# Performance work log

Hardware: AMD Instinct MI355X
Metric: run time of the kernel (lower is better)

## Reference

```python
import jax, jax.numpy as jnp
import numpy as np

B, T, H = 16, 2048, 1024
L_ORDER, R_ORDER = 1, 1
K = L_ORDER + R_ORDER + 1
THRESH = 1.0


def _alphas(hidden, conv_w, conv_b, lin_w, lin_b):
    # hidden: [B, T, H]
    context = jnp.swapaxes(hidden, 1, 2)  # [B, H, T]
    q = jnp.pad(context, ((0, 0), (0, 0), (L_ORDER, R_ORDER)))  # ConstantPad1d
    mem = jax.lax.conv_general_dilated(
        q, conv_w, (1,), 'VALID',
        dimension_numbers=('NCH', 'OIH', 'NCH'),
        feature_group_count=conv_w.shape[0])  # depthwise conv, groups=idim
    mem = mem + conv_b[None, :, None]
    out = jnp.swapaxes(mem + context, 1, 2)  # [B, T, H] (dropout = identity, eval)
    out = jax.nn.relu(out)
    out = out @ lin_w.T + lin_b  # [B, T, 1]
    return jax.nn.sigmoid(out)[..., 0]  # [B, T]


def _cif_scan(hidden, alphas, threshold):
    # sequential integrate-and-fire over time, vectorized over batch via lax.scan
    b, t, h = hidden.shape

    def step(carry, xs):
        integrate, frame = carry          # [B], [B, H]
        alpha, h_t = xs                   # [B], [B, H]
        dist = 1.0 - integrate            # distribution_completion
        integrate = integrate + alpha
        fires_t = integrate
        fire = integrate >= threshold
        integrate = jnp.where(fire, integrate - 1.0, integrate)
        cur = jnp.where(fire, dist, alpha)
        rem = alpha - cur
        frame = frame + cur[:, None] * h_t
        frames_t = frame
        frame = jnp.where(fire[:, None], rem[:, None] * h_t, frame)
        return (integrate, frame), (fires_t, frames_t)

    init = (jnp.zeros((b,), hidden.dtype), jnp.zeros((b, h), hidden.dtype))
    xs = (jnp.swapaxes(alphas, 0, 1), jnp.swapaxes(hidden, 0, 1))
    _, (fires, frames) = jax.lax.scan(step, init, xs)
    return jnp.swapaxes(frames, 0, 1), jnp.swapaxes(fires, 0, 1)  # [B,T,H], [B,T]


def _gather_fired(frames, fires, threshold, max_label_len):
    # per-batch select frames where fires>=threshold, pad to max_label_len
    b, t, h = frames.shape
    mask = fires >= threshold                         # [B, T]
    rank = jnp.cumsum(mask.astype(jnp.int32), axis=1) - 1
    idx = jnp.where(mask, rank, max_label_len)        # invalid -> dummy row
    out = jnp.zeros((b, max_label_len + 1, h), frames.dtype)
    out = out.at[jnp.arange(b)[:, None], idx].add(
        jnp.where(mask[..., None], frames, 0.0))
    return out[:, :max_label_len]


def setup_inputs() -> dict:
    key = jax.random.key(0)
    k1, k2, k3, k4 = jax.random.split(key, 4)
    hidden = jax.random.normal(k1, (B, T, H), jnp.float32)
    conv_w = jax.random.normal(k2, (H, 1, K), jnp.float32) / np.sqrt(K)
    conv_b = jax.random.normal(k3, (H,), jnp.float32) * 0.01
    lin_w = jax.random.normal(k4, (1, H), jnp.float32) / np.sqrt(H)
    lin_b = jnp.zeros((1,), jnp.float32)
    return {"hidden": hidden, "conv_w": conv_w, "conv_b": conv_b,
            "lin_w": lin_w, "lin_b": lin_b}


def reference(hidden, conv_w, conv_b, lin_w, lin_b):
    alphas = _alphas(hidden, conv_w, conv_b, lin_w, lin_b)  # [B, T]
    cif_length = alphas.sum(-1)                             # [B]
    frames, fires = _cif_scan(hidden, alphas, THRESH)
    # data-dependent output length (matches torch: round(alphas.sum(-1)).max())
    max_label_len = int(jnp.round(cif_length).astype(jnp.int32).max())
    cif_output = _gather_fired(frames, fires, THRESH, max_label_len)
    return cif_output, cif_length, fires
```

## Files before the change

### kernel.cpp

```cpp
#include <hip/hip_runtime.h>
#include <math.h>

#define B_ 16
#define T_ 2048
#define H_ 1024
#define TPB 32
#define KPB 8

typedef float f32x4_t __attribute__((ext_vector_type(4)));

__device__ __forceinline__ void ntstore4(float* p, float4 v) {
    f32x4_t w = { v.x, v.y, v.z, v.w };
    __builtin_nontemporal_store(w, (f32x4_t*)p);
}

__global__ __launch_bounds__(256) void k1_alphas(
    const float* __restrict__ hidden, const float* __restrict__ conv_w,
    const float* __restrict__ conv_b, const float* __restrict__ lin_w,
    const float* __restrict__ lin_b, float* __restrict__ alphas)
{
    const int tile = blockIdx.x & (T_ / TPB - 1);
    const int b    = blockIdx.x / (T_ / TPB);
    const int tid  = threadIdx.x;
    const int h0   = tid * 4;

    float w0[4], w1[4], w2[4];
    {
        const float4* cw = (const float4*)(conv_w + (size_t)h0 * 3);
        float4 c0 = cw[0], c1 = cw[1], c2 = cw[2];
        w0[0] = c0.x; w1[0] = c0.y; w2[0] = c0.z;
        w0[1] = c0.w; w1[1] = c1.x; w2[1] = c1.y;
        w0[2] = c1.z; w1[2] = c1.w; w2[2] = c2.x;
        w0[3] = c2.y; w1[3] = c2.z; w2[3] = c2.w;
    }
    const float4 cb = *(const float4*)(conv_b + h0);
    const float4 lw = *(const float4*)(lin_w + h0);
    const float  lb = lin_b[0];

    const size_t base = ((size_t)b * T_) * H_ + h0;
    const int t0 = tile * TPB;
    const float4 zero4 = make_float4(0.f, 0.f, 0.f, 0.f);

    float4 prev = (t0 > 0) ? *(const float4*)(hidden + base + (size_t)(t0 - 1) * H_)
                           : zero4;
    float4 curr = *(const float4*)(hidden + base + (size_t)t0 * H_);
    float4 buf0 = *(const float4*)(hidden + base + (size_t)(t0 + 1) * H_);
    float4 buf1 = *(const float4*)(hidden + base + (size_t)(t0 + 2) * H_);
    float4 buf2 = *(const float4*)(hidden + base + (size_t)(t0 + 3) * H_);
    float4 buf3 = *(const float4*)(hidden + base + (size_t)(t0 + 4) * H_);

    __shared__ float lds[4][TPB];
    const int wave = tid >> 6;
    const int lane = tid & 63;

    #pragma unroll
    for (int tt = 0; tt < TPB; ++tt) {
        float4 next;
        const int tp = t0 + tt + 5;
        switch (tt & 3) {
        case 0: next = buf0;
                buf0 = (tp < T_) ? *(const float4*)(hidden + base + (size_t)tp * H_) : zero4;
                break;
        case 1: next = buf1;
                buf1 = (tp < T_) ? *(const float4*)(hidden + base + (size_t)tp * H_) : zero4;
                break;
        case 2: next = buf2;
                buf2 = (tp < T_) ? *(const float4*)(hidden + base + (size_t)tp * H_) : zero4;
                break;
        default: next = buf3;
                buf3 = (tp < T_) ? *(const float4*)(hidden + base + (size_t)tp * H_) : zero4;
                break;
        }

        float p = 0.f, v;
        v = fmaf(w0[0], prev.x, fmaf(w1[0], curr.x, fmaf(w2[0], next.x, cb.x + curr.x)));
        p = fmaf(fmaxf(v, 0.f), lw.x, p);
        v = fmaf(w0[1], prev.y, fmaf(w1[1], curr.y, fmaf(w2[1], next.y, cb.y + curr.y)));
        p = fmaf(fmaxf(v, 0.f), lw.y, p);
        v = fmaf(w0[2], prev.z, fmaf(w1[2], curr.z, fmaf(w2[2], next.z, cb.z + curr.z)));
        p = fmaf(fmaxf(v, 0.f), lw.z, p);
        v = fmaf(w0[3], prev.w, fmaf(w1[3], curr.w, fmaf(w2[3], next.w, cb.w + curr.w)));
        p = fmaf(fmaxf(v, 0.f), lw.w, p);
        #pragma unroll
        for (int m = 32; m; m >>= 1) p += __shfl_xor(p, m);
        if (lane == 0) lds[wave][tt] = p;
        prev = curr; curr = next;
    }
    __syncthreads();
    if (tid < TPB) {
        float s = lds[0][tid] + lds[1][tid] + lds[2][tid] + lds[3][tid] + lb;
        alphas[(size_t)b * T_ + t0 + tid] = 1.f / (1.f + expf(-s));
    }
}

__global__ __launch_bounds__(256) void k2_scan_coef(
    const float* __restrict__ alphas, float* __restrict__ fires,
    float* __restrict__ wgt,
    int* __restrict__ fire_pos, int* __restrict__ n_fires,
    float* __restrict__ cif_length, int Lpad)
{
    const int b = blockIdx.x;
    const int tid = threadIdx.x;
    const size_t base = (size_t)b * T_;

    __shared__ float sA[T_];
    __shared__ float sF[T_];

    {
        const int i = tid * 8;
        *(float4*)(sA + i)     = *(const float4*)(alphas + base + i);
        *(float4*)(sA + i + 4) = *(const float4*)(alphas + base + i + 4);
    }
    __syncthreads();

    if (tid == 0) {
        float4 a0 = *(const float4*)(sA + 0);
        float4 a1 = *(const float4*)(sA + 4);
        float4 a2 = *(const float4*)(sA + 8);
        float4 a3 = *(const float4*)(sA + 12);
        float I = 0.f;
        for (int t = 0; t < T_; t += 16) {
            const int tn = (t + 16 < T_) ? t + 16 : 0;
            float4 b0 = *(const float4*)(sA + tn);
            float4 b1 = *(const float4*)(sA + tn + 4);
            float4 b2 = *(const float4*)(sA + tn + 8);
            float4 b3 = *(const float4*)(sA + tn + 12);

            float4 f0, f1, f2, f3;
            I += a0.x; f0.x = I; I = __builtin_amdgcn_fractf(I);
            I += a0.y; f0.y = I; I = __builtin_amdgcn_fractf(I);
            I += a0.z; f0.z = I; I = __builtin_amdgcn_fractf(I);
            I += a0.w; f0.w = I; I = __builtin_amdgcn_fractf(I);
            I += a1.x; f1.x = I; I = __builtin_amdgcn_fractf(I);
            I += a1.y; f1.y = I; I = __builtin_amdgcn_fractf(I);
            I += a1.z; f1.z = I; I = __builtin_amdgcn_fractf(I);
            I += a1.w; f1.w = I; I = __builtin_amdgcn_fractf(I);
            I += a2.x; f2.x = I; I = __builtin_amdgcn_fractf(I);
            I += a2.y; f2.y = I; I = __builtin_amdgcn_fractf(I);
            I += a2.z; f2.z = I; I = __builtin_amdgcn_fractf(I);
            I += a2.w; f2.w = I; I = __builtin_amdgcn_fractf(I);
            I += a3.x; f3.x = I; I = __builtin_amdgcn_fractf(I);
            I += a3.y; f3.y = I; I = __builtin_amdgcn_fractf(I);
            I += a3.z; f3.z = I; I = __builtin_amdgcn_fractf(I);
            I += a3.w; f3.w = I; I = __builtin_amdgcn_fractf(I);

            *(float4*)(sF + t)      = f0;
            *(float4*)(sF + t + 4)  = f1;
            *(float4*)(sF + t + 8)  = f2;
            *(float4*)(sF + t + 12) = f3;
            a0 = b0; a1 = b1; a2 = b2; a3 = b3;
        }
    }
    __syncthreads();

    const int t0 = tid * 8;
    float a[8], f[8];
    #pragma unroll
    for (int j = 0; j < 8; ++j) { a[j] = sA[t0 + j]; f[j] = sF[t0 + j]; }
    const float fprev = (t0 == 0) ? 0.f : sF[t0 - 1];

    ntstore4(fires + base + t0,     make_float4(f[0], f[1], f[2], f[3]));
    ntstore4(fires + base + t0 + 4, make_float4(f[4], f[5], f[6], f[7]));

    float w[16];
    bool fr[8];
    float asum = 0.f;
    int cnt = 0;
    #pragma unroll
    for (int j = 0; j < 8; ++j) {
        float fp = (j == 0) ? fprev : f[j - 1];
        float Iprev = __builtin_amdgcn_fractf(fp);
        fr[j] = (f[j] >= 1.f);
        const float dist = 1.f - Iprev;
        const float cu = fr[j] ? dist : a[j];
        const float re = a[j] - cu;
        w[2 * j]     = cu;
        w[2 * j + 1] = fr[j] ? re : -1.f;
        cnt += fr[j] ? 1 : 0;
        asum += a[j];
    }
    {
        const size_t wb = ((size_t)b * T_ + t0) * 2;
        *(float4*)(wgt + wb)      = *(float4*)(w);
        *(float4*)(wgt + wb + 4)  = *(float4*)(w + 4);
        *(float4*)(wgt + wb + 8)  = *(float4*)(w + 8);
        *(float4*)(wgt + wb + 12) = *(float4*)(w + 12);
    }

    const int lane = tid & 63, wave = tid >> 6;
    int inc = cnt;
    #pragma unroll
    for (int d = 1; d < 64; d <<= 1) {
        int v = __shfl_up(inc, d);
        if (lane >= d) inc += v;
    }
    __shared__ int wsum[4];
    if (lane == 63) wsum[wave] = inc;
    __syncthreads();
    int waveoff = 0;
    for (int w2 = 0; w2 < wave; ++w2) waveoff += wsum[w2];
    int r = waveoff + inc - cnt;
    #pragma unroll
    for (int j = 0; j < 8; ++j) {
        if (fr[j]) {
            if (r < Lpad) fire_pos[b * Lpad + r] = t0 + j;
            ++r;
        }
    }
    if (tid == 255) n_fires[b] = waveoff + inc;

    float s = asum;
    #pragma unroll
    for (int m = 32; m; m >>= 1) s += __shfl_xor(s, m);
    __shared__ float wred[4];
    if (lane == 0) wred[wave] = s;
    __syncthreads();
    if (tid == 0) cif_length[b] = wred[0] + wred[1] + wred[2] + wred[3];
}

__global__ __launch_bounds__(256) void k3_frames(
    const float* __restrict__ hidden, const float* __restrict__ wgt,
    const int* __restrict__ fire_pos, const int* __restrict__ n_fires,
    float* __restrict__ out, int L, int Lpad)
{
    const int k0 = blockIdx.x * KPB;
    const int b  = blockIdx.y;
    const int tid = threadIdx.x;
    const int h0 = tid * 4;
    const size_t hb = ((size_t)b * T_) * H_ + h0;
    const float2* wb = (const float2*)wgt + (size_t)b * T_;

    const int n = __builtin_amdgcn_readfirstlane(n_fires[b]);
    const int kmax = min(KPB, L - k0);
    const int kact = min(kmax, n - k0);

    const float4 zero4 = make_float4(0.f, 0.f, 0.f, 0.f);
    if (kact <= 0) {
        for (int kk = 0; kk < kmax; ++kk)
            ntstore4(out + ((size_t)b * L + (k0 + kk)) * H_ + h0, zero4);
        return;
    }

    const int tend = __builtin_amdgcn_readfirstlane(fire_pos[b * Lpad + k0 + kact - 1]);

    float4 acc;
    int t;
    if (k0 > 0) {
        const int s0 = __builtin_amdgcn_readfirstlane(fire_pos[b * Lpad + k0 - 1]);
        const float4 hr = *(const float4*)(hidden + hb + (size_t)s0 * H_);
        const float rm = wb[s0].y;
        acc.x = rm * hr.x; acc.y = rm * hr.y; acc.z = rm * hr.z; acc.w = rm * hr.w;
        t = s0 + 1;
    } else {
        acc = zero4;
        t = 0;
    }

    float4 hA, hB, hC, hD;
    float2 wA, wB, wC, wD;
    hA = *(const float4*)(hidden + hb + (size_t)t * H_);
    wA = wb[t];
    if (t + 1 <= tend) {
        hB = *(const float4*)(hidden + hb + (size_t)(t + 1) * H_);
        wB = wb[t + 1];
    } else { hB = zero4; wB = make_float2(0.f, -1.f); }
    if (t + 2 <= tend) {
        hC = *(const float4*)(hidden + hb + (size_t)(t + 2) * H_);
        wC = wb[t + 2];
    } else { hC = zero4; wC = make_float2(0.f, -1.f); }

    int kk = 0;
    while (t <= tend) {
        if (t + 3 <= tend) {
            hD = *(const float4*)(hidden + hb + (size_t)(t + 3) * H_);
            wD = wb[t + 3];
        } else { hD = zero4; wD = make_float2(0.f, -1.f); }

        acc.x = fmaf(wA.x, hA.x, acc.x);
        acc.y = fmaf(wA.x, hA.y, acc.y);
        acc.z = fmaf(wA.x, hA.z, acc.z);
        acc.w = fmaf(wA.x, hA.w, acc.w);
        if (wA.y >= 0.f) {
            ntstore4(out + ((size_t)b * L + (k0 + kk)) * H_ + h0, acc);
            acc.x = wA.y * hA.x; acc.y = wA.y * hA.y;
            acc.z = wA.y * hA.z; acc.w = wA.y * hA.w;
            ++kk;
        }
        hA = hB; wA = wB; hB = hC; wB = wC; hC = hD; wC = wD;
        ++t;
    }

    for (; kk < kmax; ++kk)
        ntstore4(out + ((size_t)b * L + (k0 + kk)) * H_ + h0, zero4);
}

extern "C" void kernel_launch(void* const* d_in, const int* in_sizes, int n_in,
                              void* d_out, int out_size, void* d_ws, size_t ws_size,
                              hipStream_t stream) {
    const float* hidden = (const float*)d_in[0];
    const float* conv_w = (const float*)d_in[1];
    const float* conv_b = (const float*)d_in[2];
    const float* lin_w  = (const float*)d_in[3];
    const float* lin_b  = (const float*)d_in[4];
    float* out = (float*)d_out;

    const int L = (out_size - B_ - B_ * T_) / (B_ * H_);
    float* cif_output = out;
    float* cif_length = out + (size_t)B_ * L * H_;
    float* fires      = cif_length + B_;

    float* alphas = (float*)d_ws;
    float* wgt    = alphas + (size_t)B_ * T_;
    const int Lpad = L + 8;
    int* fire_pos = (int*)(wgt + (size_t)2 * B_ * T_);
    int* n_fires  = fire_pos + (size_t)B_ * Lpad;

    k1_alphas<<<dim3(B_ * (T_ / TPB)), 256, 0, stream>>>(
        hidden, conv_w, conv_b, lin_w, lin_b, alphas);
    k2_scan_coef<<<dim3(B_), 256, 0, stream>>>(
        alphas, fires, wgt, fire_pos, n_fires, cif_length, Lpad);
    k3_frames<<<dim3((L + KPB - 1) / KPB, B_), 256, 0, stream>>>(
        hidden, wgt, fire_pos, n_fires, cif_output, L, Lpad);
}
```

Baseline: 259.7 us.

## Fuse alpha computation and scan via last-block-done atomic counter

Merges the alpha kernel and the per-batch scan kernel into one launch. Each batch's tile blocks increment an atomic counter, and the last block to finish runs the sequential scan and coefficient computation for that batch. This removes one kernel launch and the gap between the two kernels, and lets a batch's scan overlap with alpha tiles still running for other batches. In exchange it adds a memset, a fence, and a larger LDS union that every block allocates, which may lower occupancy in the alpha phase.

```diff
diff --git a/kernel.cpp b/kernel.cpp
--- a/kernel.cpp
+++ b/kernel.cpp
@@ -14,97 +14,111 @@
     __builtin_nontemporal_store(w, (f32x4_t*)p);
 }
 
-__global__ __launch_bounds__(256) void k1_alphas(
+__global__ __launch_bounds__(256) void kA_alphas_scan(
     const float* __restrict__ hidden, const float* __restrict__ conv_w,
     const float* __restrict__ conv_b, const float* __restrict__ lin_w,
-    const float* __restrict__ lin_b, float* __restrict__ alphas)
+    const float* __restrict__ lin_b,
+    float* __restrict__ alphas, float* __restrict__ fires,
+    float* __restrict__ wgt,
+    int* __restrict__ fire_pos, int* __restrict__ n_fires,
+    float* __restrict__ cif_length, int* __restrict__ cnt, int Lpad)
 {
     const int tile = blockIdx.x & (T_ / TPB - 1);
     const int b    = blockIdx.x / (T_ / TPB);
     const int tid  = threadIdx.x;
     const int h0   = tid * 4;
-
-    float w0[4], w1[4], w2[4];
-    {
-        const float4* cw = (const float4*)(conv_w + (size_t)h0 * 3);
-        float4 c0 = cw[0], c1 = cw[1], c2 = cw[2];
-        w0[0] = c0.x; w1[0] = c0.y; w2[0] = c0.z;
-        w0[1] = c0.w; w1[1] = c1.x; w2[1] = c1.y;
-        w0[2] = c1.z; w1[2] = c1.w; w2[2] = c2.x;
-        w0[3] = c2.y; w1[3] = c2.z; w2[3] = c2.w;
-    }
-    const float4 cb = *(const float4*)(conv_b + h0);
-    const float4 lw = *(const float4*)(lin_w + h0);
-    const float  lb = lin_b[0];
-
-    const size_t base = ((size_t)b * T_) * H_ + h0;
-    const int t0 = tile * TPB;
-    const float4 zero4 = make_float4(0.f, 0.f, 0.f, 0.f);
-
-    float4 prev = (t0 > 0) ? *(const float4*)(hidden + base + (size_t)(t0 - 1) * H_)
-                           : zero4;
-    float4 curr = *(const float4*)(hidden + base + (size_t)t0 * H_);
-    float4 buf0 = *(const float4*)(hidden + base + (size_t)(t0 + 1) * H_);
-    float4 buf1 = *(const float4*)(hidden + base + (size_t)(t0 + 2) * H_);
-    float4 buf2 = *(const float4*)(hidden + base + (size_t)(t0 + 3) * H_);
-    float4 buf3 = *(const float4*)(hidden + base + (size_t)(t0 + 4) * H_);
-
-    __shared__ float lds[4][TPB];
     const int wave = tid >> 6;
     const int lane = tid & 63;
 
-    #pragma unroll
-    for (int tt = 0; tt < TPB; ++tt) {
-        float4 next;
-        const int tp = t0 + tt + 5;
-        switch (tt & 3) {
-        case 0: next = buf0;
-                buf0 = (tp < T_) ? *(const float4*)(hidden + base + (size_t)tp * H_) : zero4;
-                break;
-        case 1: next = buf1;
-                buf1 = (tp < T_) ? *(const float4*)(hidden + base + (size_t)tp * H_) : zero4;
-                break;
-        case 2: next = buf2;
-                buf2 = (tp < T_) ? *(const float4*)(hidden + base + (size_t)tp * H_) : zero4;
-                break;
-        default: next = buf3;
-                buf3 = (tp < T_) ? *(const float4*)(hidden + base + (size_t)tp * H_) : zero4;
-                break;
-        }
-
-        float p = 0.f, v;
-        v = fmaf(w0[0], prev.x, fmaf(w1[0], curr.x, fmaf(w2[0], next.x, cb.x + curr.x)));
-        p = fmaf(fmaxf(v, 0.f), lw.x, p);
-        v = fmaf(w0[1], prev.y, fmaf(w1[1], curr.y, fmaf(w2[1], next.y, cb.y + curr.y)));
-        p = fmaf(fmaxf(v, 0.f), lw.y, p);
-        v = fmaf(w0[2], prev.z, fmaf(w1[2], curr.z, fmaf(w2[2], next.z, cb.z + curr.z)));
-        p = fmaf(fmaxf(v, 0.f), lw.z, p);
-        v = fmaf(w0[3], prev.w, fmaf(w1[3], curr.w, fmaf(w2[3], next.w, cb.w + curr.w)));
-        p = fmaf(fmaxf(v, 0.f), lw.w, p);
+    __shared__ union {
+        float k1lds[4][TPB];
+        struct { float sA[T_]; float sF[T_]; } k2;
+    } sh;
+    __shared__ int wsum[4];
+    __shared__ float wred[4];
+    __shared__ int amLast;
+
+    {
+        float w0[4], w1[4], w2[4];
+        {
+            const float4* cw = (const float4*)(conv_w + (size_t)h0 * 3);
+            float4 c0 = cw[0], c1 = cw[1], c2 = cw[2];
+            w0[0] = c0.x; w1[0] = c0.y; w2[0] = c0.z;
+            w0[1] = c0.w; w1[1] = c1.x; w2[1] = c1.y;
+            w0[2] = c1.z; w1[2] = c1.w; w2[2] = c2.x;
+            w0[3] = c2.y; w1[3] = c2.z; w2[3] = c2.w;
+        }
+        const float4 cb = *(const float4*)(conv_b + h0);
+        const float4 lw = *(const float4*)(lin_w + h0);
+        const float  lb = lin_b[0];
+
+        const size_t base = ((size_t)b * T_) * H_ + h0;
+        const int t0 = tile * TPB;
+        const float4 zero4 = make_float4(0.f, 0.f, 0.f, 0.f);
+
+        float4 prev = (t0 > 0) ? *(const float4*)(hidden + base + (size_t)(t0 - 1) * H_)
+                               : zero4;
+        float4 curr = *(const float4*)(hidden + base + (size_t)t0 * H_);
+        float4 buf0 = *(const float4*)(hidden + base + (size_t)(t0 + 1) * H_);
+        float4 buf1 = *(const float4*)(hidden + base + (size_t)(t0 + 2) * H_);
+        float4 buf2 = *(const float4*)(hidden + base + (size_t)(t0 + 3) * H_);
+        float4 buf3 = *(const float4*)(hidden + base + (size_t)(t0 + 4) * H_);
+
         #pragma unroll
-        for (int m = 32; m; m >>= 1) p += __shfl_xor(p, m);
-        if (lane == 0) lds[wave][tt] = p;
-        prev = curr; curr = next;
-    }
-    __syncthreads();
-    if (tid < TPB) {
-        float s = lds[0][tid] + lds[1][tid] + lds[2][tid] + lds[3][tid] + lb;
-        alphas[(size_t)b * T_ + t0 + tid] = 1.f / (1.f + expf(-s));
-    }
-}
-
-__global__ __launch_bounds__(256) void k2_scan_coef(
-    const float* __restrict__ alphas, float* __restrict__ fires,
-    float* __restrict__ wgt,
-    int* __restrict__ fire_pos, int* __restrict__ n_fires,
-    float* __restrict__ cif_length, int Lpad)
-{
-    const int b = blockIdx.x;
-    const int tid = threadIdx.x;
+        for (int tt = 0; tt < TPB; ++tt) {
+            float4 next;
+            const int tp = t0 + tt + 5;
+            switch (tt & 3) {
+            case 0: next = buf0;
+                    buf0 = (tp < T_) ? *(const float4*)(hidden + base + (size_t)tp * H_) : zero4;
+                    break;
+            case 1: next = buf1;
+                    buf1 = (tp < T_) ? *(const float4*)(hidden + base + (size_t)tp * H_) : zero4;
+                    break;
+            case 2: next = buf2;
+                    buf2 = (tp < T_) ? *(const float4*)(hidden + base + (size_t)tp * H_) : zero4;
+                    break;
+            default: next = buf3;
+                    buf3 = (tp < T_) ? *(const float4*)(hidden + base + (size_t)tp * H_) : zero4;
+                    break;
+            }
+
+            float p = 0.f, v;
+            v = fmaf(w0[0], prev.x, fmaf(w1[0], curr.x, fmaf(w2[0], next.x, cb.x + curr.x)));
+            p = fmaf(fmaxf(v, 0.f), lw.x, p);
+            v = fmaf(w0[1], prev.y, fmaf(w1[1], curr.y, fmaf(w2[1], next.y, cb.y + curr.y)));
+            p = fmaf(fmaxf(v, 0.f), lw.y, p);
+            v = fmaf(w0[2], prev.z, fmaf(w1[2], curr.z, fmaf(w2[2], next.z, cb.z + curr.z)));
+            p = fmaf(fmaxf(v, 0.f), lw.z, p);
+            v = fmaf(w0[3], prev.w, fmaf(w1[3], curr.w, fmaf(w2[3], next.w, cb.w + curr.w)));
+            p = fmaf(fmaxf(v, 0.f), lw.w, p);
+            #pragma unroll
+            for (int m = 32; m; m >>= 1) p += __shfl_xor(p, m);
+            if (lane == 0) sh.k1lds[wave][tt] = p;
+            prev = curr; curr = next;
+        }
+        __syncthreads();
+        if (tid < TPB) {
+            float s = sh.k1lds[0][tid] + sh.k1lds[1][tid] + sh.k1lds[2][tid]
+                    + sh.k1lds[3][tid] + lb;
+            const float sig = 1.f / (1.f + expf(-s));
+            __hip_atomic_store(alphas + (size_t)b * T_ + t0 + tid, sig,
+                               __ATOMIC_RELAXED, __HIP_MEMORY_SCOPE_AGENT);
+        }
+        __syncthreads();
+    }
+
+    if (tid == 0) {
+        const int prev = atomicAdd(cnt + b, 1);
+        amLast = (prev == (T_ / TPB - 1));
+        if (amLast) __threadfence();
+    }
+    __syncthreads();
+    if (!amLast) return;
+
     const size_t base = (size_t)b * T_;
-
-    __shared__ float sA[T_];
-    __shared__ float sF[T_];
+    float* sA = sh.k2.sA;
+    float* sF = sh.k2.sF;
 
     {
         const int i = tid * 8;
@@ -165,7 +179,7 @@
     float w[16];
     bool fr[8];
     float asum = 0.f;
-    int cnt = 0;
+    int cntf = 0;
     #pragma unroll
     for (int j = 0; j < 8; ++j) {
         float fp = (j == 0) ? fprev : f[j - 1];
@@ -176,7 +190,7 @@
         const float re = a[j] - cu;
         w[2 * j]     = cu;
         w[2 * j + 1] = fr[j] ? re : -1.f;
-        cnt += fr[j] ? 1 : 0;
+        cntf += fr[j] ? 1 : 0;
         asum += a[j];
     }
     {
@@ -187,19 +201,17 @@
         *(float4*)(wgt + wb + 12) = *(float4*)(w + 12);
     }
 
-    const int lane = tid & 63, wave = tid >> 6;
-    int inc = cnt;
+    int inc = cntf;
     #pragma unroll
     for (int d = 1; d < 64; d <<= 1) {
         int v = __shfl_up(inc, d);
         if (lane >= d) inc += v;
     }
-    __shared__ int wsum[4];
     if (lane == 63) wsum[wave] = inc;
     __syncthreads();
     int waveoff = 0;
     for (int w2 = 0; w2 < wave; ++w2) waveoff += wsum[w2];
-    int r = waveoff + inc - cnt;
+    int r = waveoff + inc - cntf;
     #pragma unroll
     for (int j = 0; j < 8; ++j) {
         if (fr[j]) {
@@ -212,7 +224,6 @@
     float s = asum;
     #pragma unroll
     for (int m = 32; m; m >>= 1) s += __shfl_xor(s, m);
-    __shared__ float wred[4];
     if (lane == 0) wred[wave] = s;
     __syncthreads();
     if (tid == 0) cif_length[b] = wred[0] + wred[1] + wred[2] + wred[3];
@@ -314,11 +325,12 @@
     const int Lpad = L + 8;
     int* fire_pos = (int*)(wgt + (size_t)2 * B_ * T_);
     int* n_fires  = fire_pos + (size_t)B_ * Lpad;
-
-    k1_alphas<<<dim3(B_ * (T_ / TPB)), 256, 0, stream>>>(
-        hidden, conv_w, conv_b, lin_w, lin_b, alphas);
-    k2_scan_coef<<<dim3(B_), 256, 0, stream>>>(
-        alphas, fires, wgt, fire_pos, n_fires, cif_length, Lpad);
+    int* cnt      = n_fires + B_;
+
+    hipMemsetAsync(cnt, 0, B_ * sizeof(int), stream);
+    kA_alphas_scan<<<dim3(B_ * (T_ / TPB)), 256, 0, stream>>>(
+        hidden, conv_w, conv_b, lin_w, lin_b,
+        alphas, fires, wgt, fire_pos, n_fires, cif_length, cnt, Lpad);
     k3_frames<<<dim3((L + KPB - 1) / KPB, B_), 256, 0, stream>>>(
         hidden, wgt, fire_pos, n_fires, cif_output, L, Lpad);
 }
```

New measurement: 272.5 us. 5.0% more time.
